# Performance work log

Hardware: AMD Instinct MI355X
Metric: run time of the kernel (lower is better)

The kernel has to match this reference:

```python
import jax, jax.numpy as jnp
import numpy as np

N = 100000      # nodes
E = 1600000     # edges (avg degree 16)
IN = 512        # in_channels
H = 256         # hidden_channels
L = 8           # num_layers
ALPHA = 0.1
THETA = 0.5


def setup_inputs() -> dict:
    key = jax.random.key(0)
    k0, k1, k2, k3 = jax.random.split(key, 4)
    x = jax.random.normal(k0, (N, IN), jnp.float32)
    edge_index = jax.random.randint(k1, (2, E), 0, N, dtype=jnp.int64)
    W_embed = jax.random.normal(k2, (IN, H), jnp.float32) / np.sqrt(IN)
    b_embed = jnp.zeros((H,), jnp.float32)
    W_convs = jax.random.normal(k3, (L, H, H), jnp.float32) / np.sqrt(H)
    return {"x": x, "edge_index": edge_index, "W_embed": W_embed,
            "b_embed": b_embed, "W_convs": W_convs}


def _gcn_norm(edge_index, n):
    # gcn_norm: A_hat = A + I, D^{-1/2} A_hat D^{-1/2}
    loop = jnp.arange(n, dtype=edge_index.dtype)
    row = jnp.concatenate([edge_index[0], loop])  # source
    col = jnp.concatenate([edge_index[1], loop])  # target
    ones = jnp.ones(row.shape[0], jnp.float32)
    deg = jax.ops.segment_sum(ones, col, num_segments=n)
    dinv = jnp.where(deg > 0, jax.lax.rsqrt(deg), 0.0)
    norm = dinv[row] * dinv[col]  # [E+N]
    return row, col, norm


def _propagate(x, row, col, norm, n):
    # SpMM: out[i] = sum_{(j->i)} norm_e * x[j]
    msgs = x[row] * norm[:, None]  # [E+N, H]
    return jax.ops.segment_sum(msgs, col, num_segments=n)


def _gcn2_conv(x, x0, row, col, norm, W, layer):
    beta = np.log(THETA / layer + 1.0)
    h = _propagate(x, row, col, norm, x.shape[0])
    h = (1.0 - ALPHA) * h + ALPHA * x0          # initial residual (shared_weights)
    return (1.0 - beta) * h + beta * (h @ W)    # identity mapping


def reference(x, edge_index, W_embed, b_embed, W_convs):
    n = x.shape[0]
    row, col, norm = _gcn_norm(edge_index, n)
    h = jax.nn.relu(x @ W_embed + b_embed)
    h0 = h
    for l in range(L - 1):
        h = _gcn2_conv(h, h0, row, col, norm, W_convs[l], layer=l + 1)
        h = jax.nn.relu(h)  # dropout is identity in eval mode
    h = _gcn2_conv(h, h0, row, col, norm, W_convs[L - 1], layer=L)
    return h
```

## Files before the change

### kernel.cpp

```cpp
#include <hip/hip_runtime.h>
#include <cmath>

#define NNODES 100000
#define NEDGES 1600000
#define INC 512
#define HC 256
#define NLAYERS 8

typedef _Float16 half8 __attribute__((ext_vector_type(8)));
typedef _Float16 half4v __attribute__((ext_vector_type(4)));
typedef float floatx4 __attribute__((ext_vector_type(4)));

struct __attribute__((aligned(8))) EdgeP { int s; float w; };

__global__ void k_detect(const unsigned int* __restrict__ eb, int* __restrict__ mode) {
  int lane = threadIdx.x;
  unsigned v = eb[2 * lane + 1];
  unsigned long long nz = __ballot(v != 0u);
  if (lane == 0) *mode = (nz == 0ull) ? 1 : 0;
}

__device__ __forceinline__ int edge_at(const void* eb, int m, int i) {
  return m ? (int)((const long long*)eb)[i] : ((const int*)eb)[i];
}


__global__ __launch_bounds__(256) void k_zero2(int* __restrict__ a, int* __restrict__ b, int n) {
  int i = blockIdx.x * 256 + threadIdx.x;
  if (i < n) { a[i] = 0; b[i] = 0; }
}

__global__ __launch_bounds__(256) void k_count(const void* __restrict__ eb, const int* __restrict__ mode,
                                               int* __restrict__ counts) {
  int e = blockIdx.x * 256 + threadIdx.x;
  if (e >= NEDGES) return;
  int m = *mode;
  atomicAdd(&counts[edge_at(eb, m, NEDGES + e)], 1);
}

__global__ __launch_bounds__(256) void k_dinv(const int* __restrict__ counts, float* __restrict__ dinv) {
  int i = blockIdx.x * 256 + threadIdx.x;
  if (i < NNODES) dinv[i] = 1.0f / sqrtf((float)counts[i] + 1.0f);
}

__global__ __launch_bounds__(256) void k_scan1(const int* __restrict__ counts, int* __restrict__ rowptr,
                                               int* __restrict__ partials) {
  __shared__ int sm[256];
  int i = blockIdx.x * 256 + threadIdx.x;
  int v = (i < NNODES) ? counts[i] : 0;
  sm[threadIdx.x] = v;
  __syncthreads();
  for (int off = 1; off < 256; off <<= 1) {
    int u = (threadIdx.x >= off) ? sm[threadIdx.x - off] : 0;
    __syncthreads();
    sm[threadIdx.x] += u;
    __syncthreads();
  }
  if (i < NNODES) rowptr[i] = sm[threadIdx.x] - v;
  if (threadIdx.x == 255) partials[blockIdx.x] = sm[255];
}

__global__ __launch_bounds__(512) void k_scan2(int* __restrict__ partials, int* __restrict__ rowptr, int nb) {
  __shared__ int sm[512];
  int t = threadIdx.x;
  int v = (t < nb) ? partials[t] : 0;
  sm[t] = v;
  __syncthreads();
  for (int off = 1; off < 512; off <<= 1) {
    int u = (t >= off) ? sm[t - off] : 0;
    __syncthreads();
    sm[t] += u;
    __syncthreads();
  }
  if (t < nb) partials[t] = sm[t] - v;
  if (t == 0) rowptr[NNODES] = NEDGES;
}

__global__ __launch_bounds__(256) void k_scan3(int* __restrict__ rowptr, const int* __restrict__ partials) {
  int i = blockIdx.x * 256 + threadIdx.x;
  if (i < NNODES) rowptr[i] += partials[blockIdx.x];
}

__global__ __launch_bounds__(256) void k_fill(const void* __restrict__ eb, const int* __restrict__ mode,
                                              const int* __restrict__ rowptr,
                                              int* __restrict__ cursor, const float* __restrict__ dinv,
                                              EdgeP* __restrict__ ep) {
  int e = blockIdx.x * 256 + threadIdx.x;
  if (e >= NEDGES) return;
  int m = *mode;
  int r = edge_at(eb, m, e), c = edge_at(eb, m, NEDGES + e);
  int p = rowptr[c] + atomicAdd(&cursor[c], 1);
  EdgeP pr; pr.s = r; pr.w = dinv[r] * dinv[c];
  ep[p] = pr;
}

__global__ __launch_bounds__(256) void k_tr_wemb(const float* __restrict__ W, _Float16* __restrict__ WT) {
  int idx = blockIdx.x * 256 + threadIdx.x;
  int k = idx & 511, c = idx >> 9;
  WT[idx] = (_Float16)W[k * 256 + c];
}
__global__ __launch_bounds__(256) void k_tr_wc(const float* __restrict__ W, _Float16* __restrict__ WT) {
  int idx = blockIdx.x * 256 + threadIdx.x;
  int k = idx & 255, n = (idx >> 8) & 255, l = idx >> 16;
  WT[idx] = (_Float16)W[(l * 256 + k) * 256 + n];
}


template <int K, bool AF16, bool BIAS, bool ID, bool RELU, bool F16OUT>
__global__ __launch_bounds__(256) void k_dense(const void* A, const _Float16* __restrict__ WT,
                                               const float* __restrict__ bias,
                                               const void* mfid,
                                               float ob, float beta,
                                               _Float16* __restrict__ outh, _Float16* __restrict__ outh2,
                                               float* outf) {
  int t = threadIdx.x;
  int wave = t >> 6, lane = t & 63;
  int r = lane & 15, g = lane >> 4;
  int row0 = blockIdx.x * 64;
  int c0 = wave * 64;
  int ar[4];
#pragma unroll
  for (int rt = 0; rt < 4; ++rt) {
    int rr = row0 + rt * 16 + r;
    ar[rt] = (rr < NNODES) ? rr : (NNODES - 1);
  }

  auto loadA = [&](half8 (&a)[4], int ks) {
#pragma unroll
    for (int rt = 0; rt < 4; ++rt) {
      if constexpr (AF16) {
        a[rt] = *(const half8*)((const _Float16*)A + (size_t)ar[rt] * K + ks + g * 8);
      } else {
        const float* ap = (const float*)A + (size_t)ar[rt] * K + ks + g * 8;
        float4 p0 = *(const float4*)ap;
        float4 p1 = *(const float4*)(ap + 4);
        a[rt] = half8{ (_Float16)p0.x, (_Float16)p0.y, (_Float16)p0.z, (_Float16)p0.w,
                       (_Float16)p1.x, (_Float16)p1.y, (_Float16)p1.z, (_Float16)p1.w };
      }
    }
  };
  auto loadB = [&](half8 (&b)[4], int ks) {
#pragma unroll
    for (int ct = 0; ct < 4; ++ct)
      b[ct] = *(const half8*)(WT + (size_t)(c0 + ct * 16 + r) * K + ks + g * 8);
  };

  floatx4 acc[4][4] = {};
  half8 aP[4], bP[4], aQ[4], bQ[4];
  loadA(aP, 0); loadB(bP, 0);
#pragma unroll
  for (int ks = 0; ks < K; ks += 64) {
    loadA(aQ, ks + 32); loadB(bQ, ks + 32);
#pragma unroll
    for (int rt = 0; rt < 4; ++rt)
#pragma unroll
      for (int ct = 0; ct < 4; ++ct)
        acc[rt][ct] = __builtin_amdgcn_mfma_f32_16x16x32_f16(aP[rt], bP[ct], acc[rt][ct], 0, 0, 0);
    if (ks + 64 < K) { loadA(aP, ks + 64); loadB(bP, ks + 64); }
#pragma unroll
    for (int rt = 0; rt < 4; ++rt)
#pragma unroll
      for (int ct = 0; ct < 4; ++ct)
        acc[rt][ct] = __builtin_amdgcn_mfma_f32_16x16x32_f16(aQ[rt], bQ[ct], acc[rt][ct], 0, 0, 0);
  }

  auto idval = [&](size_t off) -> float {
    if constexpr (AF16) return (float)((const _Float16*)mfid)[off];
    else return ((const float*)mfid)[off];
  };

  if constexpr (!F16OUT) {
    __syncthreads();
#pragma unroll
    for (int rt = 0; rt < 4; ++rt) {
#pragma unroll
      for (int q = 0; q < 4; ++q) {
        int row = row0 + rt * 16 + g * 4 + q;
        if (row >= NNODES) continue;
#pragma unroll
        for (int ct = 0; ct < 4; ++ct) {
          int col = c0 + ct * 16 + r;
          size_t off = (size_t)row * HC + col;
          float v = acc[rt][ct][q];
          if constexpr (ID) v = ob * idval(off) + beta * v;
          if constexpr (BIAS) v += bias[col];
          if constexpr (RELU) v = fmaxf(v, 0.0f);
          outf[off] = v;
        }
      }
    }
  } else {
    __shared__ _Float16 Cl[64][264];
#pragma unroll
    for (int rt = 0; rt < 4; ++rt) {
#pragma unroll
      for (int q = 0; q < 4; ++q) {
        int lrow = rt * 16 + g * 4 + q;
        int row = row0 + lrow;
        int crow = (row < NNODES) ? row : (NNODES - 1);
#pragma unroll
        for (int ct = 0; ct < 4; ++ct) {
          int col = c0 + ct * 16 + r;
          float v = acc[rt][ct][q];
          if constexpr (ID) v = ob * idval((size_t)crow * HC + col) + beta * v;
          if constexpr (BIAS) v += bias[col];
          if constexpr (RELU) v = fmaxf(v, 0.0f);
          Cl[lrow][col] = (_Float16)v;
        }
      }
    }
    __syncthreads();
    int lrow = t >> 2, cc = (t & 3) * 64;
    int grow = row0 + lrow;
    if (grow < NNODES) {
      size_t base = (size_t)grow * HC + cc;
#pragma unroll
      for (int i = 0; i < 8; ++i) {
        half8 v = *(const half8*)&Cl[lrow][cc + i * 8];
        *(half8*)(outh + base + i * 8) = v;
        if (outh2) *(half8*)(outh2 + base + i * 8) = v;
      }
    }
  }
}


template <bool F16OUT>
__global__ __launch_bounds__(256) void k_spmm(const _Float16* __restrict__ h, const _Float16* __restrict__ h0,
                                              const int* __restrict__ rowptr, const EdgeP* __restrict__ ep,
                                              const float* __restrict__ dinv,
                                              float* __restrict__ mf, _Float16* __restrict__ mh) {
  int wave = threadIdx.x >> 6, lane = threadIdx.x & 63;
  int node = blockIdx.x * 4 + wave;
  if (node >= NNODES) return;
  int c = lane * 4;
  size_t base = (size_t)node * HC + c;
  float di = dinv[node];
  float ws = di * di;
  half4v hv = *(const half4v*)(h + base);
  float a0 = ws * (float)hv[0], a1 = ws * (float)hv[1], a2 = ws * (float)hv[2], a3 = ws * (float)hv[3];
  int t = rowptr[node], en = rowptr[node + 1];
  for (; t + 3 < en; t += 4) {
    EdgeP p0 = ep[t], p1 = ep[t + 1], p2 = ep[t + 2], p3 = ep[t + 3];
    half4v x0 = *(const half4v*)(h + (size_t)p0.s * HC + c);
    half4v x1 = *(const half4v*)(h + (size_t)p1.s * HC + c);
    half4v x2 = *(const half4v*)(h + (size_t)p2.s * HC + c);
    half4v x3 = *(const half4v*)(h + (size_t)p3.s * HC + c);
    a0 += p0.w * (float)x0[0] + p1.w * (float)x1[0] + p2.w * (float)x2[0] + p3.w * (float)x3[0];
    a1 += p0.w * (float)x0[1] + p1.w * (float)x1[1] + p2.w * (float)x2[1] + p3.w * (float)x3[1];
    a2 += p0.w * (float)x0[2] + p1.w * (float)x1[2] + p2.w * (float)x2[2] + p3.w * (float)x3[2];
    a3 += p0.w * (float)x0[3] + p1.w * (float)x1[3] + p2.w * (float)x2[3] + p3.w * (float)x3[3];
  }
  for (; t < en; ++t) {
    EdgeP p0 = ep[t];
    half4v x0 = *(const half4v*)(h + (size_t)p0.s * HC + c);
    a0 += p0.w * (float)x0[0];
    a1 += p0.w * (float)x0[1];
    a2 += p0.w * (float)x0[2];
    a3 += p0.w * (float)x0[3];
  }
  half4v h0v = *(const half4v*)(h0 + base);
  float m0 = 0.9f * a0 + 0.1f * (float)h0v[0];
  float m1 = 0.9f * a1 + 0.1f * (float)h0v[1];
  float m2 = 0.9f * a2 + 0.1f * (float)h0v[2];
  float m3 = 0.9f * a3 + 0.1f * (float)h0v[3];
  if constexpr (F16OUT) {
    half4v mo = { (_Float16)m0, (_Float16)m1, (_Float16)m2, (_Float16)m3 };
    *(half4v*)(mh + base) = mo;
  } else {
    *(float4*)(mf + base) = make_float4(m0, m1, m2, m3);
  }
}


extern "C" void kernel_launch(void* const* d_in, const int* in_sizes, int n_in,
                              void* d_out, int out_size, void* d_ws, size_t ws_size,
                              hipStream_t stream) {
  const float* x = (const float*)d_in[0];
  const void* ei = d_in[1];
  const float* wemb = (const float*)d_in[2];
  const float* bemb = (const float*)d_in[3];
  const float* wc = (const float*)d_in[4];
  (void)in_sizes; (void)n_in; (void)out_size; (void)ws_size;

  char* ws = (char*)d_ws;
  size_t o = 0;
  auto alloc = [&](size_t bytes) -> char* {
    char* p = ws + o;
    o = (o + bytes + 511) & ~(size_t)511;
    return p;
  };
  _Float16* hh      = (_Float16*)alloc((size_t)NNODES * HC * 2);
  _Float16* h0h     = (_Float16*)alloc((size_t)NNODES * HC * 2);
  EdgeP*    ep      = (EdgeP*)alloc((size_t)NEDGES * 8);
  _Float16* wembT   = (_Float16*)alloc((size_t)INC * HC * 2);
  _Float16* wcT     = (_Float16*)alloc((size_t)NLAYERS * HC * HC * 2);
  int*      counts  = (int*)alloc((size_t)NNODES * 4);
  int*      cursor  = (int*)alloc((size_t)NNODES * 4);
  int*      rowptr  = (int*)alloc((size_t)(NNODES + 1) * 4);
  float*    dinv    = (float*)alloc((size_t)NNODES * 4);
  int*      partials= (int*)alloc(2048);
  int*      mode    = (int*)alloc(256);
  _Float16* mh      = (_Float16*)d_out;
  float*    mf      = (float*)d_out;

  const int NB = (NNODES + 255) / 256;
  const int GEMM_GRID = (NNODES + 63) / 64;

  k_detect<<<1, 64, 0, stream>>>((const unsigned int*)ei, mode);
  k_zero2<<<NB, 256, 0, stream>>>(counts, cursor, NNODES);
  k_tr_wemb<<<(INC * HC) / 256, 256, 0, stream>>>(wemb, wembT);
  k_tr_wc<<<(NLAYERS * HC * HC) / 256, 256, 0, stream>>>(wc, wcT);
  k_count<<<(NEDGES + 255) / 256, 256, 0, stream>>>(ei, mode, counts);
  k_dinv<<<NB, 256, 0, stream>>>(counts, dinv);
  k_scan1<<<NB, 256, 0, stream>>>(counts, rowptr, partials);
  k_scan2<<<1, 512, 0, stream>>>(partials, rowptr, NB);
  k_scan3<<<NB, 256, 0, stream>>>(rowptr, partials);
  k_fill<<<(NEDGES + 255) / 256, 256, 0, stream>>>(ei, mode, rowptr, cursor, dinv, ep);

  k_dense<INC, false, true, false, true, true><<<GEMM_GRID, 256, 0, stream>>>(
      x, wembT, bemb, (const void*)nullptr, 0.0f, 1.0f, hh, h0h, (float*)nullptr);

  for (int l = 0; l < NLAYERS; ++l) {
    float beta = (float)log(0.5 / (double)(l + 1) + 1.0);
    float ob = 1.0f - beta;
    bool last = (l == NLAYERS - 1);
    if (!last) {
      k_spmm<true><<<NNODES / 4, 256, 0, stream>>>(hh, h0h, rowptr, ep, dinv,
                                                   (float*)nullptr, mh);
      k_dense<HC, true, false, true, true, true><<<GEMM_GRID, 256, 0, stream>>>(
          mh, wcT + (size_t)l * HC * HC, (const float*)nullptr, mh, ob, beta,
          hh, (_Float16*)nullptr, (float*)nullptr);
    } else {
      k_spmm<false><<<NNODES / 4, 256, 0, stream>>>(hh, h0h, rowptr, ep, dinv,
                                                    mf, (_Float16*)nullptr);
      k_dense<HC, false, false, true, false, false><<<GEMM_GRID, 256, 0, stream>>>(
          mf, wcT + (size_t)l * HC * HC, (const float*)nullptr, mf, ob, beta,
          (_Float16*)nullptr, (_Float16*)nullptr, (float*)d_out);
    }
  }
}
```

Baseline: 2.063 ms.

## Fuse SpMM aggregation and dense GCNII transform into one per-layer kernel

Replaces the separate k_spmm and k_dense launches per layer with one k_layer kernel. Each block gathers 64 nodes' aggregated features into an LDS tile, then runs MFMA against the layer weight and writes the ReLU'd fp16 result into a ping-pong buffer. This removes the global write and re-read of the intermediate propagated matrix and halves the kernel launches per layer. In exchange, each wave handles 16 nodes serially, so fewer waves are in flight to hide gather latency, and each block uses about 34 KB of LDS, which limits occupancy.

```diff
diff --git a/kernel.cpp b/kernel.cpp
--- a/kernel.cpp
+++ b/kernel.cpp
@@ -225,50 +225,112 @@
 }
 
 
-template <bool F16OUT>
-__global__ __launch_bounds__(256) void k_spmm(const _Float16* __restrict__ h, const _Float16* __restrict__ h0,
-                                              const int* __restrict__ rowptr, const EdgeP* __restrict__ ep,
-                                              const float* __restrict__ dinv,
-                                              float* __restrict__ mf, _Float16* __restrict__ mh) {
-  int wave = threadIdx.x >> 6, lane = threadIdx.x & 63;
-  int node = blockIdx.x * 4 + wave;
-  if (node >= NNODES) return;
+template <bool LAST>
+__global__ __launch_bounds__(256) void k_layer(const _Float16* __restrict__ h,
+                                               const _Float16* __restrict__ h0,
+                                               const int* __restrict__ rowptr,
+                                               const EdgeP* __restrict__ ep,
+                                               const float* __restrict__ dinv,
+                                               const _Float16* __restrict__ WT,
+                                               float ob, float beta,
+                                               _Float16* __restrict__ hn, float* __restrict__ outf) {
+  __shared__ _Float16 M[64][264];
+  int t = threadIdx.x;
+  int wave = t >> 6, lane = t & 63;
+  int row0 = blockIdx.x * 64;
   int c = lane * 4;
-  size_t base = (size_t)node * HC + c;
-  float di = dinv[node];
-  float ws = di * di;
-  half4v hv = *(const half4v*)(h + base);
-  float a0 = ws * (float)hv[0], a1 = ws * (float)hv[1], a2 = ws * (float)hv[2], a3 = ws * (float)hv[3];
-  int t = rowptr[node], en = rowptr[node + 1];
-  for (; t + 3 < en; t += 4) {
-    EdgeP p0 = ep[t], p1 = ep[t + 1], p2 = ep[t + 2], p3 = ep[t + 3];
-    half4v x0 = *(const half4v*)(h + (size_t)p0.s * HC + c);
-    half4v x1 = *(const half4v*)(h + (size_t)p1.s * HC + c);
-    half4v x2 = *(const half4v*)(h + (size_t)p2.s * HC + c);
-    half4v x3 = *(const half4v*)(h + (size_t)p3.s * HC + c);
-    a0 += p0.w * (float)x0[0] + p1.w * (float)x1[0] + p2.w * (float)x2[0] + p3.w * (float)x3[0];
-    a1 += p0.w * (float)x0[1] + p1.w * (float)x1[1] + p2.w * (float)x2[1] + p3.w * (float)x3[1];
-    a2 += p0.w * (float)x0[2] + p1.w * (float)x1[2] + p2.w * (float)x2[2] + p3.w * (float)x3[2];
-    a3 += p0.w * (float)x0[3] + p1.w * (float)x1[3] + p2.w * (float)x2[3] + p3.w * (float)x3[3];
-  }
-  for (; t < en; ++t) {
-    EdgeP p0 = ep[t];
-    half4v x0 = *(const half4v*)(h + (size_t)p0.s * HC + c);
-    a0 += p0.w * (float)x0[0];
-    a1 += p0.w * (float)x0[1];
-    a2 += p0.w * (float)x0[2];
-    a3 += p0.w * (float)x0[3];
-  }
-  half4v h0v = *(const half4v*)(h0 + base);
-  float m0 = 0.9f * a0 + 0.1f * (float)h0v[0];
-  float m1 = 0.9f * a1 + 0.1f * (float)h0v[1];
-  float m2 = 0.9f * a2 + 0.1f * (float)h0v[2];
-  float m3 = 0.9f * a3 + 0.1f * (float)h0v[3];
-  if constexpr (F16OUT) {
-    half4v mo = { (_Float16)m0, (_Float16)m1, (_Float16)m2, (_Float16)m3 };
-    *(half4v*)(mh + base) = mo;
-  } else {
-    *(float4*)(mf + base) = make_float4(m0, m1, m2, m3);
+
+  for (int i = 0; i < 16; ++i) {
+    int lrow = wave * 16 + i;
+    int node = row0 + lrow;
+    if (node < NNODES) {
+      size_t base = (size_t)node * HC + c;
+      float di = dinv[node];
+      float wsw = di * di;
+      half4v hv = *(const half4v*)(h + base);
+      float a0 = wsw * (float)hv[0], a1 = wsw * (float)hv[1];
+      float a2 = wsw * (float)hv[2], a3 = wsw * (float)hv[3];
+      int e = rowptr[node], en = rowptr[node + 1];
+      for (; e + 3 < en; e += 4) {
+        EdgeP p0 = ep[e], p1 = ep[e + 1], p2 = ep[e + 2], p3 = ep[e + 3];
+        half4v x0 = *(const half4v*)(h + (size_t)p0.s * HC + c);
+        half4v x1 = *(const half4v*)(h + (size_t)p1.s * HC + c);
+        half4v x2 = *(const half4v*)(h + (size_t)p2.s * HC + c);
+        half4v x3 = *(const half4v*)(h + (size_t)p3.s * HC + c);
+        a0 += p0.w * (float)x0[0] + p1.w * (float)x1[0] + p2.w * (float)x2[0] + p3.w * (float)x3[0];
+        a1 += p0.w * (float)x0[1] + p1.w * (float)x1[1] + p2.w * (float)x2[1] + p3.w * (float)x3[1];
+        a2 += p0.w * (float)x0[2] + p1.w * (float)x1[2] + p2.w * (float)x2[2] + p3.w * (float)x3[2];
+        a3 += p0.w * (float)x0[3] + p1.w * (float)x1[3] + p2.w * (float)x2[3] + p3.w * (float)x3[3];
+      }
+      for (; e < en; ++e) {
+        EdgeP p0 = ep[e];
+        half4v x0 = *(const half4v*)(h + (size_t)p0.s * HC + c);
+        a0 += p0.w * (float)x0[0];
+        a1 += p0.w * (float)x0[1];
+        a2 += p0.w * (float)x0[2];
+        a3 += p0.w * (float)x0[3];
+      }
+      half4v h0v = *(const half4v*)(h0 + base);
+      half4v mo = { (_Float16)(0.9f * a0 + 0.1f * (float)h0v[0]),
+                    (_Float16)(0.9f * a1 + 0.1f * (float)h0v[1]),
+                    (_Float16)(0.9f * a2 + 0.1f * (float)h0v[2]),
+                    (_Float16)(0.9f * a3 + 0.1f * (float)h0v[3]) };
+      *(half4v*)&M[lrow][c] = mo;
+    } else {
+      *(half4v*)&M[lrow][c] = half4v{ (_Float16)0, (_Float16)0, (_Float16)0, (_Float16)0 };
+    }
+  }
+  __syncthreads();
+
+  int r = lane & 15, g = lane >> 4;
+  int c0 = wave * 64;
+  floatx4 acc[4][4] = {};
+#pragma unroll
+  for (int ks = 0; ks < HC; ks += 32) {
+    half8 a[4], b[4];
+#pragma unroll
+    for (int rt = 0; rt < 4; ++rt)
+      a[rt] = *(const half8*)&M[rt * 16 + r][ks + g * 8];
+#pragma unroll
+    for (int ct = 0; ct < 4; ++ct)
+      b[ct] = *(const half8*)(WT + (size_t)(c0 + ct * 16 + r) * HC + ks + g * 8);
+#pragma unroll
+    for (int rt = 0; rt < 4; ++rt)
+#pragma unroll
+      for (int ct = 0; ct < 4; ++ct)
+        acc[rt][ct] = __builtin_amdgcn_mfma_f32_16x16x32_f16(a[rt], b[ct], acc[rt][ct], 0, 0, 0);
+  }
+  __syncthreads();
+
+#pragma unroll
+  for (int rt = 0; rt < 4; ++rt) {
+#pragma unroll
+    for (int q = 0; q < 4; ++q) {
+      int lrow = rt * 16 + g * 4 + q;
+#pragma unroll
+      for (int ct = 0; ct < 4; ++ct) {
+        int col = c0 + ct * 16 + r;
+        float v = ob * (float)M[lrow][col] + beta * acc[rt][ct][q];
+        if constexpr (!LAST) {
+          v = fmaxf(v, 0.0f);
+          M[lrow][col] = (_Float16)v;
+        } else {
+          int row = row0 + lrow;
+          if (row < NNODES) outf[(size_t)row * HC + col] = v;
+        }
+      }
+    }
+  }
+  if constexpr (!LAST) {
+    __syncthreads();
+    int lrow = t >> 2, cc = (t & 3) * 64;
+    int grow = row0 + lrow;
+    if (grow < NNODES) {
+      size_t base = (size_t)grow * HC + cc;
+#pragma unroll
+      for (int i = 0; i < 8; ++i)
+        *(half8*)(hn + base + i * 8) = *(const half8*)&M[lrow][cc + i * 8];
+    }
   }
 }
 
@@ -301,8 +363,7 @@
   float*    dinv    = (float*)alloc((size_t)NNODES * 4);
   int*      partials= (int*)alloc(2048);
   int*      mode    = (int*)alloc(256);
-  _Float16* mh      = (_Float16*)d_out;
-  float*    mf      = (float*)d_out;
+  _Float16* hd      = (_Float16*)d_out;
 
   const int NB = (NNODES + 255) / 256;
   const int GEMM_GRID = (NNODES + 63) / 64;
@@ -319,24 +380,21 @@
   k_fill<<<(NEDGES + 255) / 256, 256, 0, stream>>>(ei, mode, rowptr, cursor, dinv, ep);
 
   k_dense<INC, false, true, false, true, true><<<GEMM_GRID, 256, 0, stream>>>(
-      x, wembT, bemb, (const void*)nullptr, 0.0f, 1.0f, hh, h0h, (float*)nullptr);
-
+      x, wembT, bemb, (const void*)nullptr, 0.0f, 1.0f, hd, h0h, (float*)nullptr);
+
+  _Float16* cur = hd;
+  _Float16* nxt = hh;
   for (int l = 0; l < NLAYERS; ++l) {
     float beta = (float)log(0.5 / (double)(l + 1) + 1.0);
     float ob = 1.0f - beta;
-    bool last = (l == NLAYERS - 1);
-    if (!last) {
-      k_spmm<true><<<NNODES / 4, 256, 0, stream>>>(hh, h0h, rowptr, ep, dinv,
-                                                   (float*)nullptr, mh);
-      k_dense<HC, true, false, true, true, true><<<GEMM_GRID, 256, 0, stream>>>(
-          mh, wcT + (size_t)l * HC * HC, (const float*)nullptr, mh, ob, beta,
-          hh, (_Float16*)nullptr, (float*)nullptr);
+    const _Float16* W = wcT + (size_t)l * HC * HC;
+    if (l < NLAYERS - 1) {
+      k_layer<false><<<GEMM_GRID, 256, 0, stream>>>(cur, h0h, rowptr, ep, dinv, W,
+                                                    ob, beta, nxt, (float*)nullptr);
+      _Float16* tmp = cur; cur = nxt; nxt = tmp;
     } else {
-      k_spmm<false><<<NNODES / 4, 256, 0, stream>>>(hh, h0h, rowptr, ep, dinv,
-                                                    mf, (_Float16*)nullptr);
-      k_dense<HC, false, false, true, false, false><<<GEMM_GRID, 256, 0, stream>>>(
-          mf, wcT + (size_t)l * HC * HC, (const float*)nullptr, mf, ob, beta,
-          (_Float16*)nullptr, (_Float16*)nullptr, (float*)d_out);
-    }
-  }
-}
+      k_layer<true><<<GEMM_GRID, 256, 0, stream>>>(cur, h0h, rowptr, ep, dinv, W,
+                                                   ob, beta, (_Float16*)nullptr, (float*)d_out);
+    }
+  }
+}
```

Result: slower. 2.329 ms (+12.9%).
